# Kernel tuning notes

Hardware: AMD Instinct MI355X
Metric: run time of the kernel (lower is better)

The kernel has to match this reference:

```python
import jax, jax.numpy as jnp
import numpy as np

B, C, W, H = 2, 64, 96, 96  # N = W*H = 9216 spatial positions


def conv1x1(x, w, b):
    # x: (B, Cin, W, H), w: (Cout, Cin), b: (Cout,) -> (B, Cout, W, H)
    return jnp.einsum('bchw,oc->bohw', x, w) + b[None, :, None, None]


def setup_inputs() -> dict:
    key = jax.random.key(0)
    ks = jax.random.split(key, 4)
    c8 = C // 8
    s = 0.05  # small weight scale keeps softmax logits in a sane range
    return {
        'x': jax.random.normal(ks[0], (B, C, W, H), jnp.float32),
        'wq': jax.random.normal(ks[1], (c8, C), jnp.float32) * s,
        'bq': jnp.zeros((c8,), jnp.float32),
        'wk': jax.random.normal(ks[2], (c8, C), jnp.float32) * s,
        'bk': jnp.zeros((c8,), jnp.float32),
        'wv': jax.random.normal(ks[3], (C, C), jnp.float32) * s,
        'bv': jnp.zeros((C,), jnp.float32),
        'gamma': jnp.full((1,), 0.5, jnp.float32),
    }


def reference(x, wq, bq, wk, bk, wv, bv, gamma):
    b, c, w, h = x.shape
    n = w * h
    q = conv1x1(x, wq, bq).reshape(b, -1, n)   # (B, C//8, N)
    k = conv1x1(x, wk, bk).reshape(b, -1, n)   # (B, C//8, N)
    v = conv1x1(x, wv, bv).reshape(b, c, n)    # (B, C, N)
    energy = jnp.einsum('bci,bcj->bij', q, k)  # (B, N, N)
    attn = jax.nn.softmax(energy, axis=-1)
    # torch.bmm(v, attn): out[b,c,i] = sum_j v[b,c,j] * attn[b,j,i]
    out = jnp.einsum('bcj,bji->bci', v, attn).reshape(b, c, w, h)
    return gamma * out + x
```

## Files before the change

### kernel.cpp

```cpp
#include <hip/hip_runtime.h>

using half2v  = __attribute__((ext_vector_type(2))) _Float16;
using half4   = __attribute__((ext_vector_type(4))) _Float16;
using half8   = __attribute__((ext_vector_type(8))) _Float16;
using floatx4 = __attribute__((ext_vector_type(4))) float;

constexpr int BATCH = 2;
constexpr int NPOS  = 96 * 96;
constexpr int NT    = NPOS / 16;
constexpr int NST   = NPOS / 32;

#define EXP2(x) __builtin_amdgcn_exp2f(x)
#define MFMA16(A, B, C) __builtin_amdgcn_mfma_f32_16x16x16f16(A, B, C, 0, 0, 0)
#define MFMA32(A, B, C) __builtin_amdgcn_mfma_f32_16x16x32_f16(A, B, C, 0, 0, 0)

__device__ inline half8 p8_of(floatx4 e0, floatx4 e1) {
    half2v a0 = __builtin_bit_cast(half2v,
        __builtin_amdgcn_cvt_pkrtz(EXP2(e0[0]), EXP2(e0[1])));
    half2v a1 = __builtin_bit_cast(half2v,
        __builtin_amdgcn_cvt_pkrtz(EXP2(e0[2]), EXP2(e0[3])));
    half2v a2 = __builtin_bit_cast(half2v,
        __builtin_amdgcn_cvt_pkrtz(EXP2(e1[0]), EXP2(e1[1])));
    half2v a3 = __builtin_bit_cast(half2v,
        __builtin_amdgcn_cvt_pkrtz(EXP2(e1[2]), EXP2(e1[3])));
    half8 p = {a0[0], a0[1], a1[0], a1[1], a2[0], a2[1], a3[0], a3[1]};
    return p;
}

__global__ __launch_bounds__(256) void qkv_kernel(
    const float* __restrict__ x,
    const float* __restrict__ wq, const float* __restrict__ bq,
    const float* __restrict__ wk, const float* __restrict__ bk,
    const float* __restrict__ wv, const float* __restrict__ bv,
    _Float16* __restrict__ Qf, _Float16* __restrict__ Kf,
    _Float16* __restrict__ Vf)
{
    __shared__ float W[80][64];
    __shared__ float bias[80];
    __shared__ float qs[32][9];
    __shared__ float ks[32][9];
    __shared__ _Float16 vs[32][72];
    const int tid = threadIdx.x;
    for (int idx = tid; idx < 80 * 64; idx += 256) {
        int o = idx >> 6, c = idx & 63;
        float w;
        if (o < 8)       w = wq[o * 64 + c];
        else if (o < 16) w = wk[(o - 8) * 64 + c];
        else             w = wv[(o - 16) * 64 + c];
        W[o][c] = w;
    }
    if (tid < 80) {
        float bb;
        if (tid < 8)       bb = bq[tid];
        else if (tid < 16) bb = bk[tid - 8];
        else               bb = bv[tid - 16];
        bias[tid] = bb;
    }
    __syncthreads();

    const int js = blockIdx.x;
    const int b  = blockIdx.y;
    const int part = tid >> 5;
    const int jl   = tid & 31;
    const int i    = js * 32 + jl;

    float xr[64];
    #pragma unroll
    for (int c = 0; c < 64; ++c)
        xr[c] = x[(size_t)(b * 64 + c) * NPOS + i];

    #pragma unroll
    for (int q = 0; q < 10; ++q) {
        const int o = part * 10 + q;
        float s = bias[o];
        #pragma unroll
        for (int c4 = 0; c4 < 16; ++c4) {
            float4 w4 = *(const float4*)&W[o][c4 * 4];
            s += w4.x * xr[c4*4+0] + w4.y * xr[c4*4+1]
               + w4.z * xr[c4*4+2] + w4.w * xr[c4*4+3];
        }
        if (o < 8)       qs[jl][o] = s;
        else if (o < 16) ks[jl][o - 8] = s;
        else             vs[jl][o - 16] = (_Float16)s;
    }
    __syncthreads();

    const size_t tile = (size_t)b * NST + js;
    {
        const int ct = tid >> 6, l = tid & 63;
        const int g = l >> 4, cl = l & 15;
        half8 o8;
        #pragma unroll
        for (int idx = 0; idx < 8; ++idx)
            o8[idx] = vs[8 * g + idx][16 * ct + cl];
        *(half8*)&Vf[(tile * 256 + ct * 64 + l) * 8] = o8;
    }
    if (tid < 128) {
        const int l = tid >> 1, e = tid & 1;
        const int m = l & 15, g = l >> 4;
        const int jsrc = 8 * (m >> 2) + 4 * e + (m & 3);
        constexpr float LOG2E = 1.44269504088896f;
        half4 qh;
        #pragma unroll
        for (int r = 0; r < 4; ++r)
            qh[r] = (g < 2) ? (_Float16)(qs[jsrc][4 * g + r] * LOG2E)
                            : (_Float16)0.f;
        ((half4*)Qf)[(tile * 64 + l) * 2 + e] = qh;
    } else {
        const int t = tid - 128;
        const int ht = t >> 6, l = t & 63;
        const int il = l & 15, g = l >> 4;
        const int it = js * 2 + ht;
        half4 kh;
        #pragma unroll
        for (int r = 0; r < 4; ++r) {
            if (g < 2)       kh[r] = (_Float16)ks[16 * ht + il][4 * g + r];
            else if (g == 2) kh[r] = (r < 2) ? (_Float16)1.f : (_Float16)0.f;
            else             kh[r] = (_Float16)0.f;
        }
        ((half4*)Kf)[(size_t)(b * NT + it) * 64 + l] = kh;
    }
}

template<int JSPLIT>
__global__ __launch_bounds__(256, 2) void attn_kernel(
    const _Float16* __restrict__ Qf, const _Float16* __restrict__ Kf,
    const _Float16* __restrict__ Vf,
    float* __restrict__ part, float* __restrict__ part_rs)
{
    constexpr int KSTEPS = NST / JSPLIT / 4;
    __shared__ float red[4][64][17];
    const int s   = blockIdx.x;
    const int jh  = blockIdx.y;
    const int b   = s & 1;
    const int igl = s >> 1;
    const int tid = threadIdx.x;
    const int w = tid >> 6, l = tid & 63;
    const int it0 = igl * 4, i0 = igl * 64;

    const half8* __restrict__ qfb = (const half8*)Qf + (size_t)b * NST * 64;
    const half4* __restrict__ kfb = (const half4*)Kf + (size_t)b * NT * 64;
    const half8* __restrict__ vfb = (const half8*)Vf + (size_t)b * NST * 256;

    half4 kf[4];
    #pragma unroll
    for (int st = 0; st < 4; ++st) kf[st] = kfb[(size_t)(it0 + st) * 64 + l];

    half8 vones;
    #pragma unroll
    for (int e = 0; e < 8; ++e)
        vones[e] = (_Float16)(((l & 15) == 0) ? 1.f : 0.f);

    floatx4 acc[4][4];
    floatx4 rs[4];
    #pragma unroll
    for (int st = 0; st < 4; ++st) {
        rs[st] = (floatx4){0.f, 0.f, 0.f, 0.f};
        #pragma unroll
        for (int ct = 0; ct < 4; ++ct)
            acc[st][ct] = (floatx4){0.f, 0.f, 0.f, 0.f};
    }

    const floatx4 z = {0.f, 0.f, 0.f, 0.f};

    #define ASTEP(QV, V0, V1, V2, V3) do { \
        half4 qe0 = __builtin_shufflevector(QV, QV, 0, 1, 2, 3); \
        half4 qe1 = __builtin_shufflevector(QV, QV, 4, 5, 6, 7); \
        _Pragma("unroll") \
        for (int st = 0; st < 4; ++st) { \
            floatx4 e0 = MFMA16(qe0, kf[st], z); \
            floatx4 e1 = MFMA16(qe1, kf[st], z); \
            half8 p = p8_of(e0, e1); \
            acc[st][0] = MFMA32(V0, p, acc[st][0]); \
            acc[st][1] = MFMA32(V1, p, acc[st][1]); \
            acc[st][2] = MFMA32(V2, p, acc[st][2]); \
            acc[st][3] = MFMA32(V3, p, acc[st][3]); \
            rs[st]     = MFMA32(vones, p, rs[st]); \
        } \
    } while (0)

    const int st0 = jh * (NST / JSPLIT);
    const half8* qpw = qfb + (size_t)(st0 + w) * 64 + l;
    const half8* vpw = vfb + (size_t)(st0 + w) * 256 + l;

    half8 qv = qpw[0];
    half8 v0 = vpw[0], v1 = vpw[64], v2 = vpw[128], v3 = vpw[192];
    for (int k = 0; k < KSTEPS - 1; ++k) {
        const size_t nx = (size_t)(k + 1);
        half8 qn  = qpw[nx * 256];
        half8 v0n = vpw[nx * 1024],       v1n = vpw[nx * 1024 + 64];
        half8 v2n = vpw[nx * 1024 + 128], v3n = vpw[nx * 1024 + 192];
        ASTEP(qv, v0, v1, v2, v3);
        qv = qn; v0 = v0n; v1 = v1n; v2 = v2n; v3 = v3n;
    }
    ASTEP(qv, v0, v1, v2, v3);
    #undef ASTEP

    float* __restrict__ P  = part    + (size_t)jh * ((size_t)BATCH * 64 * NPOS);
    float* __restrict__ Pr = part_rs + (size_t)jh * ((size_t)BATCH * NPOS);
    #pragma unroll
    for (int st = 0; st < 4; ++st) {
        __syncthreads();
        #pragma unroll
        for (int ct = 0; ct < 4; ++ct)
            #pragma unroll
            for (int r = 0; r < 4; ++r)
                red[w][l][ct * 4 + r] = acc[st][ct][r];
        red[w][l][16] = rs[st][0];
        __syncthreads();
        const int iq = i0 + 16 * st + (l & 15);
        #pragma unroll
        for (int r = 0; r < 4; ++r) {
            float v = red[0][l][w*4+r] + red[1][l][w*4+r]
                    + red[2][l][w*4+r] + red[3][l][w*4+r];
            int c = 16 * w + 4 * (l >> 4) + r;
            size_t o = ((size_t)(b * 64 + c)) * NPOS + iq;
            P[o] = v;
        }
        if (w == 0 && l < 16) {
            float rsv = red[0][l][16] + red[1][l][16]
                      + red[2][l][16] + red[3][l][16];
            Pr[(size_t)b * NPOS + i0 + 16 * st + l] = rsv;
        }
    }
}

template<int JSPLIT>
__global__ __launch_bounds__(256) void combine_kernel(
    const float* __restrict__ part, const float* __restrict__ part_rs,
    const float* __restrict__ x, const float* __restrict__ gamma,
    float* __restrict__ out)
{
    const float g = gamma[0];
    const size_t idx = (size_t)blockIdx.x * 256 + threadIdx.x;
    const size_t stride  = ((size_t)BATCH * 64 * NPOS) / 4;
    const size_t rstride = ((size_t)BATCH * NPOS) / 4;
    const int i4 = (int)(idx % (NPOS / 4));
    const int b  = (int)(idx / ((size_t)64 * (NPOS / 4)));
    const float4* p0 = (const float4*)part;
    const float4* r0 = (const float4*)part_rs;

    float4 a = p0[idx];
    float4 rsum = r0[(size_t)b * (NPOS / 4) + i4];
    #pragma unroll
    for (int u = 1; u < JSPLIT; ++u) {
        float4 q = p0[idx + (size_t)u * stride];
        a.x += q.x; a.y += q.y; a.z += q.z; a.w += q.w;
        float4 rq = r0[(size_t)b * (NPOS / 4) + i4 + (size_t)u * rstride];
        rsum.x += rq.x; rsum.y += rq.y; rsum.z += rq.z; rsum.w += rq.w;
    }
    float4 xv = ((const float4*)x)[idx];
    float4 o;
    o.x = g * (a.x / rsum.x) + xv.x;
    o.y = g * (a.y / rsum.y) + xv.y;
    o.z = g * (a.z / rsum.z) + xv.z;
    o.w = g * (a.w / rsum.w) + xv.w;
    ((float4*)out)[idx] = o;
}

extern "C" void kernel_launch(void* const* d_in, const int* in_sizes, int n_in,
                              void* d_out, int out_size, void* d_ws, size_t ws_size,
                              hipStream_t stream)
{
    const float* x     = (const float*)d_in[0];
    const float* wq    = (const float*)d_in[1];
    const float* bq    = (const float*)d_in[2];
    const float* wk    = (const float*)d_in[3];
    const float* bk    = (const float*)d_in[4];
    const float* wv    = (const float*)d_in[5];
    const float* bv    = (const float*)d_in[6];
    const float* gamma = (const float*)d_in[7];
    float* out = (float*)d_out;

    char* wsb = (char*)d_ws;
    _Float16* Qf = (_Float16*)wsb;
    _Float16* Kf = (_Float16*)(wsb + 589824);
    _Float16* Vf = (_Float16*)(wsb + 1179648);
    float*    Pp = (float*)(wsb + 3538944);

    qkv_kernel<<<dim3(NST, BATCH), 256, 0, stream>>>(
        x, wq, bq, wk, bk, wv, bv, Qf, Kf, Vf);

    const size_t partBytes = (size_t)BATCH * 64 * NPOS * sizeof(float);
    const size_t rsBytes   = (size_t)BATCH * NPOS * sizeof(float);
    const size_t need4 = 3538944 + 4 * (partBytes + rsBytes);
    const int nblk = (BATCH * 64 * NPOS / 4) / 256;

    if (ws_size >= need4) {
        float* Prs = (float*)(wsb + 3538944 + 4 * partBytes);
        attn_kernel<4><<<dim3(NST, 4), 256, 0, stream>>>(Qf, Kf, Vf, Pp, Prs);
        combine_kernel<4><<<nblk, 256, 0, stream>>>(Pp, Prs, x, gamma, out);
    } else {
        float* Prs = (float*)(wsb + 3538944 + 2 * partBytes);
        attn_kernel<2><<<dim3(NST, 2), 256, 0, stream>>>(Qf, Kf, Vf, Pp, Prs);
        combine_kernel<2><<<nblk, 256, 0, stream>>>(Pp, Prs, x, gamma, out);
    }
}
```

Baseline: 127.1 us.

## Share softmax P tiles through LDS so each wave owns a channel slice

After: 123.8 us. -2.5%, faster.

```diff
diff --git a/kernel.cpp b/kernel.cpp
--- a/kernel.cpp
+++ b/kernel.cpp
@@ -123,13 +123,14 @@
 }
 
 template<int JSPLIT>
-__global__ __launch_bounds__(256, 2) void attn_kernel(
+__global__ __launch_bounds__(256, 3) void attn_kernel(
     const _Float16* __restrict__ Qf, const _Float16* __restrict__ Kf,
     const _Float16* __restrict__ Vf,
     float* __restrict__ part, float* __restrict__ part_rs)
 {
-    constexpr int KSTEPS = NST / JSPLIT / 4;
-    __shared__ float red[4][64][17];
+    constexpr int NSTEP = NST / JSPLIT / 4;
+    __shared__ half8 Pb[2][4][4][64];
+    __shared__ float rsred[4][4][16];
     const int s   = blockIdx.x;
     const int jh  = blockIdx.y;
     const int b   = s & 1;
@@ -151,75 +152,77 @@
     for (int e = 0; e < 8; ++e)
         vones[e] = (_Float16)(((l & 15) == 0) ? 1.f : 0.f);
 
-    floatx4 acc[4][4];
+    floatx4 acc[4];
     floatx4 rs[4];
     #pragma unroll
     for (int st = 0; st < 4; ++st) {
-        rs[st] = (floatx4){0.f, 0.f, 0.f, 0.f};
-        #pragma unroll
-        for (int ct = 0; ct < 4; ++ct)
-            acc[st][ct] = (floatx4){0.f, 0.f, 0.f, 0.f};
+        acc[st] = (floatx4){0.f, 0.f, 0.f, 0.f};
+        rs[st]  = (floatx4){0.f, 0.f, 0.f, 0.f};
     }
 
     const floatx4 z = {0.f, 0.f, 0.f, 0.f};
-
-    #define ASTEP(QV, V0, V1, V2, V3) do { \
-        half4 qe0 = __builtin_shufflevector(QV, QV, 0, 1, 2, 3); \
-        half4 qe1 = __builtin_shufflevector(QV, QV, 4, 5, 6, 7); \
-        _Pragma("unroll") \
-        for (int st = 0; st < 4; ++st) { \
-            floatx4 e0 = MFMA16(qe0, kf[st], z); \
-            floatx4 e1 = MFMA16(qe1, kf[st], z); \
-            half8 p = p8_of(e0, e1); \
-            acc[st][0] = MFMA32(V0, p, acc[st][0]); \
-            acc[st][1] = MFMA32(V1, p, acc[st][1]); \
-            acc[st][2] = MFMA32(V2, p, acc[st][2]); \
-            acc[st][3] = MFMA32(V3, p, acc[st][3]); \
-            rs[st]     = MFMA32(vones, p, rs[st]); \
-        } \
-    } while (0)
-
     const int st0 = jh * (NST / JSPLIT);
-    const half8* qpw = qfb + (size_t)(st0 + w) * 64 + l;
-    const half8* vpw = vfb + (size_t)(st0 + w) * 256 + l;
-
-    half8 qv = qpw[0];
-    half8 v0 = vpw[0], v1 = vpw[64], v2 = vpw[128], v3 = vpw[192];
-    for (int k = 0; k < KSTEPS - 1; ++k) {
-        const size_t nx = (size_t)(k + 1);
-        half8 qn  = qpw[nx * 256];
-        half8 v0n = vpw[nx * 1024],       v1n = vpw[nx * 1024 + 64];
-        half8 v2n = vpw[nx * 1024 + 128], v3n = vpw[nx * 1024 + 192];
-        ASTEP(qv, v0, v1, v2, v3);
-        qv = qn; v0 = v0n; v1 = v1n; v2 = v2n; v3 = v3n;
-    }
-    ASTEP(qv, v0, v1, v2, v3);
-    #undef ASTEP
+
+    half8 qv = qfb[(size_t)(st0 + w) * 64 + l];
+
+    for (int k = 0; k < NSTEP; ++k) {
+        const int t4 = st0 + k * 4;
+        const int buf = k & 1;
+        half8 v0 = vfb[(size_t)(t4 + 0) * 256 + w * 64 + l];
+        half8 v1 = vfb[(size_t)(t4 + 1) * 256 + w * 64 + l];
+        half8 v2 = vfb[(size_t)(t4 + 2) * 256 + w * 64 + l];
+        half8 v3 = vfb[(size_t)(t4 + 3) * 256 + w * 64 + l];
+
+        {
+            half4 qe0 = __builtin_shufflevector(qv, qv, 0, 1, 2, 3);
+            half4 qe1 = __builtin_shufflevector(qv, qv, 4, 5, 6, 7);
+            #pragma unroll
+            for (int st = 0; st < 4; ++st) {
+                floatx4 e0 = MFMA16(qe0, kf[st], z);
+                floatx4 e1 = MFMA16(qe1, kf[st], z);
+                half8 p = p8_of(e0, e1);
+                rs[st] = MFMA32(vones, p, rs[st]);
+                Pb[buf][w][st][l] = p;
+            }
+        }
+        if (k + 1 < NSTEP)
+            qv = qfb[(size_t)(st0 + (k + 1) * 4 + w) * 64 + l];
+
+        __syncthreads();
+
+        #pragma unroll
+        for (int st = 0; st < 4; ++st) {
+            acc[st] = MFMA32(v0, Pb[buf][0][st][l], acc[st]);
+            acc[st] = MFMA32(v1, Pb[buf][1][st][l], acc[st]);
+            acc[st] = MFMA32(v2, Pb[buf][2][st][l], acc[st]);
+            acc[st] = MFMA32(v3, Pb[buf][3][st][l], acc[st]);
+        }
+    }
 
     float* __restrict__ P  = part    + (size_t)jh * ((size_t)BATCH * 64 * NPOS);
     float* __restrict__ Pr = part_rs + (size_t)jh * ((size_t)BATCH * NPOS);
-    #pragma unroll
-    for (int st = 0; st < 4; ++st) {
-        __syncthreads();
-        #pragma unroll
-        for (int ct = 0; ct < 4; ++ct)
+    {
+        const int iq = i0 + (l & 15);
+        #pragma unroll
+        for (int st = 0; st < 4; ++st)
             #pragma unroll
-            for (int r = 0; r < 4; ++r)
-                red[w][l][ct * 4 + r] = acc[st][ct][r];
-        red[w][l][16] = rs[st][0];
-        __syncthreads();
-        const int iq = i0 + 16 * st + (l & 15);
-        #pragma unroll
-        for (int r = 0; r < 4; ++r) {
-            float v = red[0][l][w*4+r] + red[1][l][w*4+r]
-                    + red[2][l][w*4+r] + red[3][l][w*4+r];
-            int c = 16 * w + 4 * (l >> 4) + r;
-            size_t o = ((size_t)(b * 64 + c)) * NPOS + iq;
-            P[o] = v;
-        }
-        if (w == 0 && l < 16) {
-            float rsv = red[0][l][16] + red[1][l][16]
-                      + red[2][l][16] + red[3][l][16];
+            for (int r = 0; r < 4; ++r) {
+                int c = 16 * w + 4 * (l >> 4) + r;
+                size_t o = ((size_t)(b * 64 + c)) * NPOS + iq + 16 * st;
+                P[o] = acc[st][r];
+            }
+    }
+
+    if (l < 16) {
+        #pragma unroll
+        for (int st = 0; st < 4; ++st) rsred[w][st][l] = rs[st][0];
+    }
+    __syncthreads();
+    if (w == 0 && l < 16) {
+        #pragma unroll
+        for (int st = 0; st < 4; ++st) {
+            float rsv = rsred[0][st][l] + rsred[1][st][l]
+                      + rsred[2][st][l] + rsred[3][st][l];
             Pr[(size_t)b * NPOS + i0 + 16 * st + l] = rsv;
         }
     }
```
